# Kernel optimization log

Hardware: AMD Instinct MI355X
Metric: run time of the kernel (lower is better)

The kernel has to match this reference:

```python
import jax, jax.numpy as jnp
import numpy as np

B, T_ENC, FEAT, H, W2V, T_DEC, V = 32, 80, 4096, 256, 256, 30, 32000


def lstm_cell(x, h, c, w_ih, w_hh, b_ih, b_hh):
    # PyTorch LSTMCell: gates order i, f, g, o
    g = x @ w_ih.T + h @ w_hh.T + b_ih + b_hh
    i, f, gg, o = jnp.split(g, 4, axis=-1)
    c_new = jax.nn.sigmoid(f) * c + jax.nn.sigmoid(i) * jnp.tanh(gg)
    h_new = jax.nn.sigmoid(o) * jnp.tanh(c_new)
    return h_new, c_new


def setup_inputs() -> dict:
    key = jax.random.key(0)
    ks = jax.random.split(key, 13)
    s = 0.05
    return {
        'feat': jax.random.normal(ks[0], (B, T_ENC, FEAT), jnp.float32),
        'caption': jax.random.normal(ks[1], (B, T_DEC, W2V), jnp.float32),
        'caption_one_hot': jax.random.normal(ks[2], (B, T_DEC, V), jnp.float32),
        'keep_rate': 1,
        'w_ih1': jax.random.normal(ks[3], (4 * H, FEAT), jnp.float32) * s,
        'w_hh1': jax.random.normal(ks[4], (4 * H, H), jnp.float32) * s,
        'b_ih1': jax.random.normal(ks[5], (4 * H,), jnp.float32) * s,
        'b_hh1': jax.random.normal(ks[6], (4 * H,), jnp.float32) * s,
        'w_ih2': jax.random.normal(ks[7], (4 * H, H + W2V), jnp.float32) * s,
        'w_hh2': jax.random.normal(ks[8], (4 * H, H), jnp.float32) * s,
        'b_ih2': jax.random.normal(ks[9], (4 * H,), jnp.float32) * s,
        'b_hh2': jax.random.normal(ks[10], (4 * H,), jnp.float32) * s,
        'w_out': jax.random.normal(ks[11], (V, H), jnp.float32) * s,
        'b_out': jax.random.normal(ks[12], (V,), jnp.float32) * s,
    }


def reference(feat, caption, caption_one_hot, keep_rate,
              w_ih1, w_hh1, b_ih1, b_hh1,
              w_ih2, w_hh2, b_ih2, b_hh2,
              w_out, b_out):
    zeros_h = jnp.zeros((B, H), feat.dtype)
    pad1 = jnp.zeros((B, FEAT), feat.dtype)

    # ---------------- encoder: 80 steps ----------------
    def enc_step(carry, x_t):
        h1, c1, h2, c2 = carry
        h1, c1 = lstm_cell(x_t, h1, c1, w_ih1, w_hh1, b_ih1, b_hh1)
        h2, c2 = lstm_cell(jnp.concatenate([zeros_h, h1], axis=1), h2, c2,
                           w_ih2, w_hh2, b_ih2, b_hh2)
        return (h1, c1, h2, c2), h2

    (h1, c1, h2, c2), enc_h2 = jax.lax.scan(
        enc_step, (zeros_h, zeros_h, zeros_h, zeros_h),
        jnp.transpose(feat, (1, 0, 2)))
    enc_h2 = jnp.transpose(enc_h2, (1, 0, 2))  # [B, 80, H]

    # ---------------- decoder: teacher forcing (coin>=100 never fires) ----
    targets = jnp.argmax(caption_one_hot, axis=-1)  # [B, T_DEC]

    def dec_step(carry, xs):
        h1, c1, h2, c2, loss = carry
        word_t, tgt_t = xs  # [B, W2V], [B]
        h1, c1 = lstm_cell(pad1, h1, c1, w_ih1, w_hh1, b_ih1, b_hh1)
        h2n, c2 = lstm_cell(jnp.concatenate([word_t, h1], axis=1), h2, c2,
                            w_ih2, w_hh2, b_ih2, b_hh2)
        logits = h2n @ w_out.T + b_out  # [B, V]
        logp = jax.nn.log_softmax(logits, axis=-1)
        ce = -jnp.take_along_axis(logp, tgt_t[:, None], axis=1)[:, 0]
        loss = loss + jnp.mean(ce) / B  # sum(mean-CE)/batch, per original
        # attention: scores of encoder h2 states against current h2
        attn = jax.nn.softmax(jnp.einsum('bsh,bh->bs', enc_h2, h2n), axis=-1)
        ctx = jnp.einsum('bs,bsh->bh', attn, enc_h2)  # replaces h2 for next step
        return (h1, c1, ctx, c2, loss), None

    xs = (jnp.transpose(caption[:, :T_DEC - 1, :], (1, 0, 2)),
          jnp.transpose(targets[:, 1:T_DEC], (1, 0)))
    (h1, c1, h2, c2, total_loss), _ = jax.lax.scan(
        dec_step, (h1, c1, h2, c2, jnp.float32(0.0)), xs)
    return total_loss
```

## Files before the change

### kernel.cpp

```cpp
#include <hip/hip_runtime.h>
#include <hip/hip_bf16.h>
#include <math.h>

#define BB 32
#define TE 80
#define FEAT 4096
#define HH 256
#define W2V 256
#define TD 30
#define VV 32000
#define G4 1024

typedef unsigned short u16;
typedef unsigned int u32;
using f32x4 = __attribute__((ext_vector_type(4))) float;
using bf16x8 = __attribute__((ext_vector_type(8))) short;
using f16x2 = __attribute__((ext_vector_type(2))) _Float16;

#define SENT 0xFFFFFFFFu
#define NANF 0x7FC00000u

__device__ __forceinline__ float sigm(float x) { return 1.0f / (1.0f + expf(-x)); }
__device__ __forceinline__ u16 f2bf(float f) {
  u32 u = __float_as_uint(f);
  u32 r = (u + 0x7FFFu + ((u >> 16) & 1u)) >> 16;
  return (u16)r;
}
__device__ __forceinline__ u32 packh2(float lo, float hi) {
  f16x2 v = {(_Float16)lo, (_Float16)hi};
  return __builtin_bit_cast(u32, v);
}

#define AT_LOAD(p)     __hip_atomic_load((p), __ATOMIC_RELAXED, __HIP_MEMORY_SCOPE_AGENT)
#define AT_STORE(p, v) __hip_atomic_store((p), (v), __ATOMIC_RELAXED, __HIP_MEMORY_SCOPE_AGENT)

__device__ __forceinline__ float fdot2h(f16x2 a, f16x2 b, float c) {
#if __has_builtin(__builtin_amdgcn_fdot2)
  return __builtin_amdgcn_fdot2(a, b, c, false);
#else
  return c + (float)a[0] * (float)b[0] + (float)a[1] * (float)b[1];
#endif
}

__global__ __launch_bounds__(256) void prep_kernel(
    const float* __restrict__ feat, const float* __restrict__ w_ih1,
    const float* __restrict__ w_ih2, const float* __restrict__ caption,
    const float* __restrict__ onehot,
    const float* __restrict__ b_ih1, const float* __restrict__ b_hh1,
    const float* __restrict__ b_ih2, const float* __restrict__ b_hh2,
    u16* __restrict__ featb, u16* __restrict__ w_ih1b,
    float* __restrict__ XW2,
    float* __restrict__ bias1, float* __restrict__ bias2,
    u32* __restrict__ H1H, u32* __restrict__ H2H, u32* __restrict__ A2P,
    float* __restrict__ loss, int* __restrict__ ctrs,
    int* __restrict__ targets) {
  __shared__ __align__(16) char psm[50688];
  int blk = blockIdx.x, tid = threadIdx.x;
  if (blk < 928) {
    int k = blk;
    int s = (k >> 5) + 1, b = k & 31;
    const float* row = &onehot[((size_t)b * TD + s) * VV];
    float bv = -INFINITY;
    int bi = 0x7fffffff;
    for (int v = tid; v < VV; v += 256) {
      float x = row[v];
      if (x > bv || (x == bv && v < bi)) { bv = x; bi = v; }
    }
    float* sv = (float*)psm;
    int* si = (int*)(psm + 1024);
    sv[tid] = bv; si[tid] = bi;
    __syncthreads();
    for (int off = 128; off; off >>= 1) {
      if (tid < off) {
        float ov = sv[tid + off]; int oi = si[tid + off];
        if (ov > sv[tid] || (ov == sv[tid] && oi < si[tid])) { sv[tid] = ov; si[tid] = oi; }
      }
      __syncthreads();
    }
    if (tid == 0) targets[k] = si[0];
  } else if (blk < 3488) {
    int i0 = (blk - 928) * 1024 + tid;
#pragma unroll
    for (int ii = 0; ii < 4; ++ii) {
      int i = i0 + ii * 256;
      float4 v = *(const float4*)&feat[(size_t)i * 4];
      *(ushort4*)&featb[(size_t)i * 4] =
          make_ushort4(f2bf(v.x), f2bf(v.y), f2bf(v.z), f2bf(v.w));
    }
  } else if (blk < 4512) {
    int i0 = (blk - 3488) * 1024 + tid;
#pragma unroll
    for (int ii = 0; ii < 4; ++ii) {
      int i = i0 + ii * 256;
      float4 v = *(const float4*)&w_ih1[(size_t)i * 4];
      *(ushort4*)&w_ih1b[(size_t)i * 4] =
          make_ushort4(f2bf(v.x), f2bf(v.y), f2bf(v.z), f2bf(v.w));
    }
  } else if (blk < 4976) {
    int k = blk - 4512, nb = k & 15, t = k >> 4;
    u16* As = (u16*)psm;
    u16* Bs = (u16*)(psm + 16896);
    int nBase = nb * 64;
#pragma unroll
    for (int it = 0; it < 4; ++it) {
      int i = it * 256 + tid;
      int r = i >> 5, c8 = i & 31;
      const float* src = &caption[((size_t)r * TD + t) * 256 + c8 * 8];
      float4 v0 = *(const float4*)src;
      float4 v1 = *(const float4*)(src + 4);
      u16* dst = &As[r * 264 + c8 * 8];
      *(ushort4*)dst = make_ushort4(f2bf(v0.x), f2bf(v0.y), f2bf(v0.z), f2bf(v0.w));
      *(ushort4*)(dst + 4) = make_ushort4(f2bf(v1.x), f2bf(v1.y), f2bf(v1.z), f2bf(v1.w));
    }
#pragma unroll
    for (int it = 0; it < 8; ++it) {
      int i = it * 256 + tid;
      int r = i >> 5, c8 = i & 31;
      const float* src = &w_ih2[(size_t)(nBase + r) * 512 + c8 * 8];
      float4 v0 = *(const float4*)src;
      float4 v1 = *(const float4*)(src + 4);
      u16* dst = &Bs[r * 264 + c8 * 8];
      *(ushort4*)dst = make_ushort4(f2bf(v0.x), f2bf(v0.y), f2bf(v0.z), f2bf(v0.w));
      *(ushort4*)(dst + 4) = make_ushort4(f2bf(v1.x), f2bf(v1.y), f2bf(v1.z), f2bf(v1.w));
    }
    __syncthreads();
    int lane = tid & 63, w = tid >> 6;
    int lrow = lane & 15, lk = (lane >> 4) * 8;
    f32x4 acc[2];
    acc[0] = (f32x4){0.f, 0.f, 0.f, 0.f};
    acc[1] = (f32x4){0.f, 0.f, 0.f, 0.f};
#pragma unroll
    for (int ks = 0; ks < 8; ++ks) {
      bf16x8 bfr = *(const bf16x8*)&Bs[(w * 16 + lrow) * 264 + ks * 32 + lk];
#pragma unroll
      for (int m = 0; m < 2; ++m) {
        bf16x8 af = *(const bf16x8*)&As[(m * 16 + lrow) * 264 + ks * 32 + lk];
        acc[m] = __builtin_amdgcn_mfma_f32_16x16x32_bf16(af, bfr, acc[m], 0, 0, 0);
      }
    }
    int col = nBase + w * 16 + (lane & 15);
    float bv = b_ih2[col] + b_hh2[col];
    int orow = (lane >> 4) * 4;
#pragma unroll
    for (int m = 0; m < 2; ++m)
#pragma unroll
      for (int qq = 0; qq < 4; ++qq) {
        int bb = m * 16 + orow + qq;
        XW2[((size_t)t * 32 + bb) * G4 + col] = acc[m][qq] + bv;
      }
  } else if (blk < 5416) {
    int i = (blk - 4976) * 256 + tid;
    uint4 z = {0u, 0u, 0u, 0u};
    uint4 s = {SENT, SENT, SENT, SENT};
    uint4 v = (i < 1024) ? z : s;
    ((uint4*)H1H)[i] = v;
    ((uint4*)H2H)[i] = v;
  } else if (blk < 6296) {
    int i0 = (blk - 5416) * 1024 + tid;
    uint4 s = {NANF, NANF, NANF, NANF};
#pragma unroll
    for (int ii = 0; ii < 4; ++ii) ((uint4*)A2P)[i0 + ii * 256] = s;
  } else {
    for (int i = tid; i < 1024; i += 256) {
      bias1[i] = b_ih1[i] + b_hh1[i];
      bias2[i] = b_ih2[i] + b_hh2[i];
    }
    if (tid == 0) { *loss = 0.0f; ctrs[0] = 0; ctrs[32] = 0; }
  }
}

struct RP {
  const float *XW2, *bias1, *bias2;
  const u16 *featb, *w_ih1b;
  const float *w_hh1, *w_ih2, *w_hh2;
  u32* H1H;
  u32* H2H;
  u32* A2P;
  u16* H2NB;
};

__global__ __launch_bounds__(512, 1) void recurrent_kernel(RP p) {
  __shared__ __align__(16) char smem[133120];
  int bid = blockIdx.x, tid = threadIdx.x;
  bool isL1 = bid < 128;
  int lb = isL1 ? bid : bid - 128;
  int b = lb >> 2, q = lb & 3;
  int r2 = tid >> 1, half = tid & 1;
  int g = r2 >> 6, jj = r2 & 63;
  int grow = (g << 8) + (q << 6) + jj;

  if (isL1) {
    u16* As = (u16*)smem;
    u16* Bs = (u16*)(smem + 11520);
    float* X1L = (float*)(smem + 48384);
    f16x2* hS = (f16x2*)(smem + 130624);
    float* gb = (float*)(smem + 131136);
    float* hnew = (float*)(smem + 132160);
    {
      int lane = tid & 63, w = tid >> 6;
      int lrow = lane & 15, lk = (lane >> 4) * 8;
      f32x4 acc[5][2];
#pragma unroll
      for (int m = 0; m < 5; ++m)
#pragma unroll
        for (int n = 0; n < 2; ++n) acc[m][n] = (f32x4){0.f, 0.f, 0.f, 0.f};
      for (int k0 = 0; k0 < FEAT; k0 += 64) {
        for (int f = tid; f < 640; f += 512) {
          int r = f >> 3, c8 = f & 7;
          *(uint4*)&As[r * 72 + c8 * 8] =
              *(const uint4*)&p.featb[((size_t)(b * 80 + r)) * FEAT + k0 + c8 * 8];
        }
#pragma unroll
        for (int it = 0; it < 4; ++it) {
          int f = it * 512 + tid;
          int r = f >> 3, c8 = f & 7;
          int gg = r >> 6, u = r & 63;
          *(uint4*)&Bs[r * 72 + c8 * 8] =
              *(const uint4*)&p.w_ih1b[((size_t)(gg * 256 + q * 64 + u)) * FEAT + k0 + c8 * 8];
        }
        __syncthreads();
#pragma unroll
        for (int ks = 0; ks < 2; ++ks) {
          bf16x8 bfr[2];
#pragma unroll
          for (int n = 0; n < 2; ++n)
// ... 44 lines not shown
      b1v2 = p.bias1[512 + (q << 6) + tid];
      b1v3 = p.bias1[768 + (q << 6) + tid];
    }
    for (int T = 0; T <= 109; ++T) {
      float x0 = b1v0, x1 = b1v1, x2 = b1v2, x3 = b1v3;
      if (tid < 64 && T < TE) {
        x0 = X1L[T * 257 + tid];
        x1 = X1L[T * 257 + 64 + tid];
        x2 = X1L[T * 257 + 128 + tid];
        x3 = X1L[T * 257 + 192 + tid];
      }
      if (tid < 128) {
        const u32* src = &p.H1H[((size_t)T * 32 + b) * 128 + tid];
        u32 v = AT_LOAD(src);
        int gd = 0;
        while (v == SENT && ++gd < (1 << 24)) {
          __builtin_amdgcn_s_sleep(1);
          v = AT_LOAD(src);
        }
        hS[tid] = __builtin_bit_cast(f16x2, v);
      }
      __syncthreads();
      float a1 = 0.f, a2 = 0.f;
      {
        const uint4* hv = ((const uint4*)hS) + half * 16;
#pragma unroll
        for (int k = 0; k < 16; ++k) {
          uint4 uu = hv[k];
          f16x2 e0 = __builtin_bit_cast(f16x2, uu.x), e1 = __builtin_bit_cast(f16x2, uu.y);
          f16x2 e2 = __builtin_bit_cast(f16x2, uu.z), e3 = __builtin_bit_cast(f16x2, uu.w);
          a1 = fdot2h(e0, wA[k * 4 + 0], a1);
          a2 = fdot2h(e0, wB[k * 4 + 0], a2);
          a1 = fdot2h(e1, wA[k * 4 + 1], a1);
          a2 = fdot2h(e1, wB[k * 4 + 1], a2);
          a1 = fdot2h(e2, wA[k * 4 + 2], a1);
          a2 = fdot2h(e2, wB[k * 4 + 2], a2);
          a1 = fdot2h(e3, wA[k * 4 + 3], a1);
          a2 = fdot2h(e3, wB[k * 4 + 3], a2);
        }
      }
      a1 += __shfl_xor(a1, 1);
      a2 += __shfl_xor(a2, 1);
      if (half == 0) {
        gb[r2] = a1;
        if (T >= 1)
          AT_STORE(&p.A2P[((size_t)T * 32 + b) * 1024 + grow], __float_as_uint(a2));
      }
      __syncthreads();
      if (T <= 108) {
        if (tid < 64) {
          float gi = gb[tid] + x0;
          float gf = gb[64 + tid] + x1;
          float gG = gb[128 + tid] + x2;
          float go = gb[192 + tid] + x3;
          c1 = sigm(gf) * c1 + sigm(gi) * tanhf(gG);
          hnew[tid] = sigm(go) * tanhf(c1);
        }
        if (tid < 32) {
          u32 pk = packh2(hnew[2 * tid], hnew[2 * tid + 1]);
          AT_STORE(&p.H1H[((size_t)(T + 1) * 32 + b) * 128 + (q << 5) + tid], pk);
        }
      }
    }
  } else {
    f16x2* encLh = (f16x2*)smem;
    u16* g2Lh = (u16*)(smem + 42240);
    f16x2* hS = (f16x2*)(smem + 84480);
    float* a2pS = (float*)(smem + 85536);
    float* gb = (float*)(smem + 86560);
    float* hnew = (float*)(smem + 87584);
    float* ps = (float*)(smem + 87840);
    float* sc = (float*)(smem + 89120);
    float* red = (float*)(smem + 89440);
    f16x2 wC[64];
    {
      const float4* sC = (const float4*)(p.w_hh2 + (size_t)grow * 256 + half * 128);
#pragma unroll
      for (int k = 0; k < 32; ++k) {
        float4 u = sC[k];
        wC[k * 2 + 0] = f16x2{(_Float16)u.x, (_Float16)u.y};
        wC[k * 2 + 1] = f16x2{(_Float16)u.z, (_Float16)u.w};
      }
    }
    float c2 = 0.f;
    float b2v0 = 0, b2v1 = 0, b2v2 = 0, b2v3 = 0;
    if (tid < 64) {
      b2v0 = p.bias2[(q << 6) + tid];
      b2v1 = p.bias2[256 + (q << 6) + tid];
      b2v2 = p.bias2[512 + (q << 6) + tid];
      b2v3 = p.bias2[768 + (q << 6) + tid];
    }
    for (int U = 1; U <= 109; ++U) {
      float x0 = b2v0, x1 = b2v1, x2 = b2v2, x3 = b2v3;
      if (tid < 64 && U >= 81) {
        const float* xb = &p.XW2[((size_t)(U - 81) * 32 + b) * G4 + (q << 6) + tid];
        x0 = xb[0]; x1 = xb[256]; x2 = xb[512]; x3 = xb[768];
      }
      if (tid < 128) {
        const u32* src = &p.H2H[((size_t)(U - 1) * 32 + b) * 128 + tid];
        u32 v = AT_LOAD(src);
        int gd = 0;
        while (v == SENT && ++gd < (1 << 26)) v = AT_LOAD(src);
        f16x2 hp = __builtin_bit_cast(f16x2, v);
        hS[tid] = hp;
        if (U >= 2 && U <= 81) encLh[(U - 2) * 132 + tid] = hp;
      } else if (tid < 384) {
        int rr = tid - 128;
        int growp = ((rr >> 6) << 8) + (q << 6) + (rr & 63);
        const u32* src = &p.A2P[((size_t)U * 32 + b) * 1024 + growp];
        u32 v = AT_LOAD(src);
        int gd = 0;
        while (v == NANF && ++gd < (1 << 24)) {
          __builtin_amdgcn_s_sleep(1);
          v = AT_LOAD(src);
        }
        a2pS[rr] = __uint_as_float(v);
      }
      __syncthreads();
      float a2p0 = 0, a2p1 = 0, a2p2 = 0, a2p3 = 0;
      if (tid < 64) {
        a2p0 = a2pS[tid]; a2p1 = a2pS[64 + tid];
        a2p2 = a2pS[128 + tid]; a2p3 = a2pS[192 + tid];
      }
      if (U <= 81) {
        float a2 = 0.f;
        const uint4* hv = ((const uint4*)hS) + half * 16;
#pragma unroll
        for (int k = 0; k < 16; ++k) {
          uint4 uu = hv[k];
          a2 = fdot2h(__builtin_bit_cast(f16x2, uu.x), wC[k * 4 + 0], a2);
          a2 = fdot2h(__builtin_bit_cast(f16x2, uu.y), wC[k * 4 + 1], a2);
          a2 = fdot2h(__builtin_bit_cast(f16x2, uu.z), wC[k * 4 + 2], a2);
          a2 = fdot2h(__builtin_bit_cast(f16x2, uu.w), wC[k * 4 + 3], a2);
        }
        a2 += __shfl_xor(a2, 1);
        if (half == 0) {
          gb[r2] = a2;
          if (U >= 2) g2Lh[(U - 2) * 264 + r2] = __builtin_bit_cast(u16, (_Float16)a2);
        }
        __syncthreads();
      } else {
        if (tid < 320) {
          int t = tid >> 2, kq = tid & 3;
          float a = 0.f;
          const f16x2* e = &encLh[t * 132];
#pragma unroll
          for (int i = 0; i < 32; ++i)
            a = fdot2h(e[kq + 4 * i], hS[kq + 4 * i], a);
          ps[tid] = a;
        }
        __syncthreads();
        float sco = 0.f;
        if (tid < TE) sco = ps[4 * tid] + ps[4 * tid + 1] + ps[4 * tid + 2] + ps[4 * tid + 3];
        float av = (tid < TE) ? sco : -INFINITY;
#pragma unroll
        for (int d = 32; d; d >>= 1) av = fmaxf(av, __shfl_xor(av, d));
        if (tid == 0) red[0] = av;
        if (tid == 64) red[1] = av;
        __syncthreads();
        float m = fmaxf(red[0], red[1]);
        float e2 = (tid < TE) ? expf(sco - m) : 0.f;
        float sv = e2;
#pragma unroll
// ... 11 lines not shown
          float g2v = (float)__builtin_bit_cast(_Float16, g2Lh[t * 264 + r2]);
          acc = fmaf(sc[t], g2v, acc);
        }
        acc += __shfl_xor(acc, 1);
        if (half == 0) gb[r2] = acc;
        __syncthreads();
      }
      if (tid < 64) {
        float gi = gb[tid] + a2p0 + x0;
        float gf = gb[64 + tid] + a2p1 + x1;
        float gG = gb[128 + tid] + a2p2 + x2;
        float go = gb[192 + tid] + a2p3 + x3;
        c2 = sigm(gf) * c2 + sigm(gi) * tanhf(gG);
        float h = sigm(go) * tanhf(c2);
        hnew[tid] = h;
        if (U >= 81)
          p.H2NB[((size_t)(U - 81) * 32 + b) * 256 + (q << 6) + tid] = f2bf(h);
      }
      if (tid < 32) {
        u32 pk = packh2(hnew[2 * tid], hnew[2 * tid + 1]);
        AT_STORE(&p.H2H[((size_t)U * 32 + b) * 128 + (q << 5) + tid], pk);
      }
    }
  }
}

__global__ __launch_bounds__(256, 1) void logits_final_kernel(
    const u16* __restrict__ H2NB, const float* __restrict__ w_out,
    const float* __restrict__ b_out, const int* __restrict__ targets,
    u32* __restrict__ pmaxA, u32* __restrict__ psumA, u32* __restrict__ tgtv,
    float* __restrict__ loss, int* __restrict__ ctrs, float* __restrict__ out) {
  __shared__ __align__(16) u16 bS[32768];
  __shared__ __align__(16) u16 aS[32 * 264];
  __shared__ int tS[32];
  __shared__ float sm[256];
  int tid = threadIdx.x, bid = blockIdx.x;
#pragma unroll
  for (int it = 0; it < 16; ++it) {
    int id = it * 256 + tid;
    int nt = id >> 9, rr = (id >> 5) & 15, kg = id & 31;
    int n = bid * 128 + nt * 16 + rr;
    const float* src = &w_out[(size_t)n * 256 + kg * 8];
    float4 v0 = *(const float4*)src;
    float4 v1 = *(const float4*)(src + 4);
    u16* dst = &bS[(size_t)((nt * 32 + kg) * 16 + rr) * 8];
    *(ushort4*)dst = make_ushort4(f2bf(v0.x), f2bf(v0.y), f2bf(v0.z), f2bf(v0.w));
    *(ushort4*)(dst + 4) = make_ushort4(f2bf(v1.x), f2bf(v1.y), f2bf(v1.z), f2bf(v1.w));
  }
  int wid = tid >> 6, lane = tid & 63, lcol = lane & 15, lk = lane >> 4;
  float bo[2];
#pragma unroll
  for (int n = 0; n < 2; ++n) bo[n] = b_out[(bid * 8 + wid * 2 + n) * 16 + lcol];

  for (int rg = 0; rg < 29; ++rg) {
    __syncthreads();
    for (int i = tid; i < 1024; i += 256) {
      int r = i >> 5, c8 = i & 31;
      *(uint4*)&aS[r * 264 + c8 * 8] =
          *(const uint4*)&H2NB[(size_t)rg * 8192 + r * 256 + c8 * 8];
    }
    if (tid < 32) tS[tid] = targets[rg * 32 + tid];
    __syncthreads();
    f32x4 acc[2][2];
#pragma unroll
    for (int m = 0; m < 2; ++m)
#pragma unroll
      for (int n = 0; n < 2; ++n) acc[m][n] = (f32x4){0.f, 0.f, 0.f, 0.f};
#pragma unroll
    for (int ks = 0; ks < 8; ++ks) {
      bf16x8 a0 = *(const bf16x8*)&aS[lcol * 264 + ks * 32 + lk * 8];
      bf16x8 a1 = *(const bf16x8*)&aS[(16 + lcol) * 264 + ks * 32 + lk * 8];
      bf16x8 b0 = *(const bf16x8*)&bS[(wid * 2) * 4096 + ((ks * 4 + lk) * 16 + lcol) * 8];
      bf16x8 b1 = *(const bf16x8*)&bS[(wid * 2 + 1) * 4096 + ((ks * 4 + lk) * 16 + lcol) * 8];
      acc[0][0] = __builtin_amdgcn_mfma_f32_16x16x32_bf16(a0, b0, acc[0][0], 0, 0, 0);
      acc[0][1] = __builtin_amdgcn_mfma_f32_16x16x32_bf16(a0, b1, acc[0][1], 0, 0, 0);
      acc[1][0] = __builtin_amdgcn_mfma_f32_16x16x32_bf16(a1, b0, acc[1][0], 0, 0, 0);
      acc[1][1] = __builtin_amdgcn_mfma_f32_16x16x32_bf16(a1, b1, acc[1][1], 0, 0, 0);
    }
    int nbase = (bid * 8 + wid * 2) * 16 + lcol;
#pragma unroll
    for (int m = 0; m < 2; ++m) {
      float pm[4], psv[4];
#pragma unroll
      for (int qq = 0; qq < 4; ++qq) {
        float v0 = acc[m][0][qq] + bo[0];
        float v1 = acc[m][1][qq] + bo[1];
        int r = m * 16 + lk * 4 + qq;
        int tg = tS[r];
        if (tg == nbase) AT_STORE(&tgtv[rg * 32 + r], __float_as_uint(v0));
        if (tg == nbase + 16) AT_STORE(&tgtv[rg * 32 + r], __float_as_uint(v1));
        float mx = fmaxf(v0, v1);
#pragma unroll
        for (int d = 1; d < 16; d <<= 1) mx = fmaxf(mx, __shfl_xor(mx, d));
        float e = expf(v0 - mx) + expf(v1 - mx);
#pragma unroll
        for (int d = 1; d < 16; d <<= 1) e += __shfl_xor(e, d);
        pm[qq] = mx;
        psv[qq] = e;
      }
      if (lcol == 0) {
        int chunk = bid * 4 + wid;
#pragma unroll
        for (int qq = 0; qq < 4; ++qq) {
          int r2 = rg * 32 + m * 16 + lk * 4 + qq;
          AT_STORE(&pmaxA[(size_t)r2 * 1000 + chunk], __float_as_uint(pm[qq]));
          AT_STORE(&psumA[(size_t)r2 * 1000 + chunk], __float_as_uint(psv[qq]));
        }
      }
    }
  }
  asm volatile("s_waitcnt vmcnt(0)" ::: "memory");
  __syncthreads();
  if (tid == 0) {
    __hip_atomic_fetch_add(&ctrs[0], 1, __ATOMIC_RELEASE, __HIP_MEMORY_SCOPE_AGENT);
    int gd = 0;
    while (__hip_atomic_load(&ctrs[0], __ATOMIC_ACQUIRE, __HIP_MEMORY_SCOPE_AGENT) < 250 &&
           ++gd < (1 << 26))
      __builtin_amdgcn_s_sleep(2);
  }
  __syncthreads();
#pragma unroll
  for (int k = 0; k < 4; ++k) {
    int row = bid * 4 + k;
    if (row < 928) {
      const u32* pm = pmaxA + (size_t)row * 1000;
      const u32* psv = psumA + (size_t)row * 1000;
      float m = -INFINITY;
      for (int c = tid; c < 1000; c += 256) m = fmaxf(m, __uint_as_float(AT_LOAD(&pm[c])));
      sm[tid] = m;
      __syncthreads();
      for (int off = 128; off; off >>= 1) {
        if (tid < off) sm[tid] = fmaxf(sm[tid], sm[tid + off]);
        __syncthreads();
      }
      float M = sm[0];
      __syncthreads();
      float s = 0.f;
      for (int c = tid; c < 1000; c += 256)
        s += __uint_as_float(AT_LOAD(&psv[c])) * expf(__uint_as_float(AT_LOAD(&pm[c])) - M);
      sm[tid] = s;
      __syncthreads();
      for (int off = 128; off; off >>= 1) {
        if (tid < off) sm[tid] += sm[tid + off];
        __syncthreads();
      }
      if (tid == 0) {
        float tv = __uint_as_float(AT_LOAD(&tgtv[row]));
        atomicAdd(loss, (M + logf(sm[0]) - tv) * (1.0f / 1024.0f));
      }
      __syncthreads();
    }
  }
  asm volatile("s_waitcnt vmcnt(0)" ::: "memory");
  if (tid == 0) {
    int old = __hip_atomic_fetch_add(&ctrs[32], 1, __ATOMIC_ACQ_REL, __HIP_MEMORY_SCOPE_AGENT);
    if (old == 249) out[0] = __uint_as_float(AT_LOAD((u32*)loss));
  }
}

extern "C" void kernel_launch(void* const* d_in, const int* in_sizes, int n_in,
                              void* d_out, int out_size, void* d_ws, size_t ws_size,
                              hipStream_t stream) {
  (void)in_sizes; (void)n_in; (void)out_size; (void)ws_size;
  const float* feat    = (const float*)d_in[0];
  const float* caption = (const float*)d_in[1];
  const float* onehot  = (const float*)d_in[2];
  const float* w_ih1   = (const float*)d_in[4];
  const float* w_hh1   = (const float*)d_in[5];
  const float* b_ih1   = (const float*)d_in[6];
  const float* b_hh1   = (const float*)d_in[7];
  const float* w_ih2   = (const float*)d_in[8];
  const float* w_hh2   = (const float*)d_in[9];
  const float* b_ih2   = (const float*)d_in[10];
  const float* b_hh2   = (const float*)d_in[11];
  const float* w_out   = (const float*)d_in[12];
  const float* b_out   = (const float*)d_in[13];

  char* p = (char*)d_ws;
  auto alloc = [&](size_t bytes) {
    char* r = p;
    p += (bytes + 255) & ~(size_t)255;
    return r;
  };
  float* XW2     = (float*)alloc(29ull * 32 * 1024 * 4);
  float* bias1   = (float*)alloc(1024 * 4);
  float* bias2   = (float*)alloc(1024 * 4);
  u32*   H1H     = (u32*)alloc(110ull * 32 * 128 * 4);
  u32*   H2H     = (u32*)alloc(110ull * 32 * 128 * 4);
  u32*   A2P     = (u32*)alloc(110ull * 32 * 1024 * 4);
  u16*   H2NB    = (u16*)alloc(29ull * 8192 * 2);
  u32*   pmaxA   = (u32*)alloc(928ull * 1000 * 4);
  u32*   psumA   = (u32*)alloc(928ull * 1000 * 4);
  u32*   tgtv    = (u32*)alloc(928 * 4);
  float* lossacc = (float*)alloc(256);
  int*   ctrs    = (int*)alloc(256);
  int*   targets = (int*)alloc(29 * 32 * 4);
  u16*   featb   = (u16*)alloc(2560ull * 4096 * 2);
  u16*   w_ih1b  = (u16*)alloc(1024ull * 4096 * 2);

  prep_kernel<<<6297, 256, 0, stream>>>(
      feat, w_ih1, w_ih2, caption, onehot,
      b_ih1, b_hh1, b_ih2, b_hh2,
      featb, w_ih1b, XW2,
      bias1, bias2, H1H, H2H, A2P, lossacc, ctrs, targets);

  RP rp;
  rp.XW2 = XW2; rp.bias1 = bias1; rp.bias2 = bias2;
  rp.featb = featb; rp.w_ih1b = w_ih1b;
  rp.w_hh1 = w_hh1; rp.w_ih2 = w_ih2; rp.w_hh2 = w_hh2;
  rp.H1H = H1H; rp.H2H = H2H; rp.A2P = A2P; rp.H2NB = H2NB;
  void* args[] = {&rp};
  hipLaunchCooperativeKernel((const void*)recurrent_kernel, dim3(256), dim3(512),
                             args, 0, stream);

  logits_final_kernel<<<250, 256, 0, stream>>>(H2NB, w_out, b_out, targets,
                                               pmaxA, psumA, tgtv, lossacc, ctrs,
                                               (float*)d_out);
}
```

Measured before the change: 704.1 us.

## Fuse argmax, input projections and logits into the cooperative recurrent mega-kernel

Folds the target argmax, the caption input projection (XW2), the feature bf16 conversion and the logits/log-softmax stage into the persistent cooperative kernel. The logits now run per step while the decoder is still progressing, driven by work queues and per-step counters. The A2P exchange is halved by packing two values as fp16 pairs, and the prep kernel shrinks to weight conversion and buffer initialisation. This removes a separate kernel launch, the featb round trip through global memory and the serial tail after the recurrence. In exchange it adds spin-wait dependencies and per-block work inside the recurrent kernel, which can delay the critical-path timesteps.

```diff
diff --git a/kernel.cpp b/kernel.cpp
--- a/kernel.cpp
+++ b/kernel.cpp
@@ -18,7 +18,7 @@
 using f16x2 = __attribute__((ext_vector_type(2))) _Float16;
 
 #define SENT 0xFFFFFFFFu
-#define NANF 0x7FC00000u
+#define GUARD (1 << 22)
 
 __device__ __forceinline__ float sigm(float x) { return 1.0f / (1.0f + expf(-x)); }
 __device__ __forceinline__ u16 f2bf(float f) {
@@ -30,9 +30,13 @@
   f16x2 v = {(_Float16)lo, (_Float16)hi};
   return __builtin_bit_cast(u32, v);
 }
+__device__ __forceinline__ u32 packbf2(float lo, float hi) {
+  return (u32)f2bf(lo) | ((u32)f2bf(hi) << 16);
+}
 
 #define AT_LOAD(p)     __hip_atomic_load((p), __ATOMIC_RELAXED, __HIP_MEMORY_SCOPE_AGENT)
 #define AT_STORE(p, v) __hip_atomic_store((p), (v), __ATOMIC_RELAXED, __HIP_MEMORY_SCOPE_AGENT)
+#define AT_ADD(p, v)   __hip_atomic_fetch_add((p), (v), __ATOMIC_RELAXED, __HIP_MEMORY_SCOPE_AGENT)
 
 __device__ __forceinline__ float fdot2h(f16x2 a, f16x2 b, float c) {
 #if __has_builtin(__builtin_amdgcn_fdot2)
@@ -42,53 +46,24 @@
 #endif
 }
 
+#define C_BAR 0
+#define C_WRT 32
+#define C_ARGQ 64
+#define C_ARGD 72
+#define C_CHQ 96
+#define C_RG 128
+
 __global__ __launch_bounds__(256) void prep_kernel(
-    const float* __restrict__ feat, const float* __restrict__ w_ih1,
-    const float* __restrict__ w_ih2, const float* __restrict__ caption,
-    const float* __restrict__ onehot,
+    const float* __restrict__ w_ih1,
     const float* __restrict__ b_ih1, const float* __restrict__ b_hh1,
     const float* __restrict__ b_ih2, const float* __restrict__ b_hh2,
-    u16* __restrict__ featb, u16* __restrict__ w_ih1b,
-    float* __restrict__ XW2,
+    u16* __restrict__ w_ih1b,
     float* __restrict__ bias1, float* __restrict__ bias2,
     u32* __restrict__ H1H, u32* __restrict__ H2H, u32* __restrict__ A2P,
-    float* __restrict__ loss, int* __restrict__ ctrs,
-    int* __restrict__ targets) {
-  __shared__ __align__(16) char psm[50688];
+    float* __restrict__ loss, int* __restrict__ ctrs) {
   int blk = blockIdx.x, tid = threadIdx.x;
-  if (blk < 928) {
-    int k = blk;
-    int s = (k >> 5) + 1, b = k & 31;
-    const float* row = &onehot[((size_t)b * TD + s) * VV];
-    float bv = -INFINITY;
-    int bi = 0x7fffffff;
-    for (int v = tid; v < VV; v += 256) {
-      float x = row[v];
-      if (x > bv || (x == bv && v < bi)) { bv = x; bi = v; }
-    }
-    float* sv = (float*)psm;
-    int* si = (int*)(psm + 1024);
-    sv[tid] = bv; si[tid] = bi;
-    __syncthreads();
-    for (int off = 128; off; off >>= 1) {
-      if (tid < off) {
-        float ov = sv[tid + off]; int oi = si[tid + off];
-        if (ov > sv[tid] || (ov == sv[tid] && oi < si[tid])) { sv[tid] = ov; si[tid] = oi; }
-      }
-      __syncthreads();
-    }
-    if (tid == 0) targets[k] = si[0];
-  } else if (blk < 3488) {
-    int i0 = (blk - 928) * 1024 + tid;
-#pragma unroll
-    for (int ii = 0; ii < 4; ++ii) {
-      int i = i0 + ii * 256;
-      float4 v = *(const float4*)&feat[(size_t)i * 4];
-      *(ushort4*)&featb[(size_t)i * 4] =
-          make_ushort4(f2bf(v.x), f2bf(v.y), f2bf(v.z), f2bf(v.w));
-    }
-  } else if (blk < 4512) {
-    int i0 = (blk - 3488) * 1024 + tid;
+  if (blk < 1024) {
+    int i0 = blk * 1024 + tid;
 #pragma unroll
     for (int ii = 0; ii < 4; ++ii) {
       int i = i0 + ii * 256;
@@ -96,68 +71,16 @@
       *(ushort4*)&w_ih1b[(size_t)i * 4] =
           make_ushort4(f2bf(v.x), f2bf(v.y), f2bf(v.z), f2bf(v.w));
     }
-  } else if (blk < 4976) {
-    int k = blk - 4512, nb = k & 15, t = k >> 4;
-    u16* As = (u16*)psm;
-    u16* Bs = (u16*)(psm + 16896);
-    int nBase = nb * 64;
-#pragma unroll
-    for (int it = 0; it < 4; ++it) {
-      int i = it * 256 + tid;
-      int r = i >> 5, c8 = i & 31;
-      const float* src = &caption[((size_t)r * TD + t) * 256 + c8 * 8];
-      float4 v0 = *(const float4*)src;
-      float4 v1 = *(const float4*)(src + 4);
-      u16* dst = &As[r * 264 + c8 * 8];
-      *(ushort4*)dst = make_ushort4(f2bf(v0.x), f2bf(v0.y), f2bf(v0.z), f2bf(v0.w));
-      *(ushort4*)(dst + 4) = make_ushort4(f2bf(v1.x), f2bf(v1.y), f2bf(v1.z), f2bf(v1.w));
-    }
-#pragma unroll
-    for (int it = 0; it < 8; ++it) {
-      int i = it * 256 + tid;
-      int r = i >> 5, c8 = i & 31;
-      const float* src = &w_ih2[(size_t)(nBase + r) * 512 + c8 * 8];
-      float4 v0 = *(const float4*)src;
-      float4 v1 = *(const float4*)(src + 4);
-      u16* dst = &Bs[r * 264 + c8 * 8];
-      *(ushort4*)dst = make_ushort4(f2bf(v0.x), f2bf(v0.y), f2bf(v0.z), f2bf(v0.w));
-      *(ushort4*)(dst + 4) = make_ushort4(f2bf(v1.x), f2bf(v1.y), f2bf(v1.z), f2bf(v1.w));
-    }
-    __syncthreads();
-    int lane = tid & 63, w = tid >> 6;
-    int lrow = lane & 15, lk = (lane >> 4) * 8;
-    f32x4 acc[2];
-    acc[0] = (f32x4){0.f, 0.f, 0.f, 0.f};
-    acc[1] = (f32x4){0.f, 0.f, 0.f, 0.f};
-#pragma unroll
-    for (int ks = 0; ks < 8; ++ks) {
-      bf16x8 bfr = *(const bf16x8*)&Bs[(w * 16 + lrow) * 264 + ks * 32 + lk];
-#pragma unroll
-      for (int m = 0; m < 2; ++m) {
-        bf16x8 af = *(const bf16x8*)&As[(m * 16 + lrow) * 264 + ks * 32 + lk];
-        acc[m] = __builtin_amdgcn_mfma_f32_16x16x32_bf16(af, bfr, acc[m], 0, 0, 0);
-      }
-    }
-    int col = nBase + w * 16 + (lane & 15);
-    float bv = b_ih2[col] + b_hh2[col];
-    int orow = (lane >> 4) * 4;
-#pragma unroll
-    for (int m = 0; m < 2; ++m)
-#pragma unroll
-      for (int qq = 0; qq < 4; ++qq) {
-        int bb = m * 16 + orow + qq;
-        XW2[((size_t)t * 32 + bb) * G4 + col] = acc[m][qq] + bv;
-      }
-  } else if (blk < 5416) {
-    int i = (blk - 4976) * 256 + tid;
+  } else if (blk < 1464) {
+    int i = (blk - 1024) * 256 + tid;
     uint4 z = {0u, 0u, 0u, 0u};
     uint4 s = {SENT, SENT, SENT, SENT};
     uint4 v = (i < 1024) ? z : s;
     ((uint4*)H1H)[i] = v;
     ((uint4*)H2H)[i] = v;
-  } else if (blk < 6296) {
-    int i0 = (blk - 5416) * 1024 + tid;
-    uint4 s = {NANF, NANF, NANF, NANF};
+  } else if (blk < 1904) {
+    int i0 = (blk - 1464) * 1024 + tid;
+    uint4 s = {SENT, SENT, SENT, SENT};
 #pragma unroll
     for (int ii = 0; ii < 4; ++ii) ((uint4*)A2P)[i0 + ii * 256] = s;
   } else {
@@ -165,21 +88,118 @@
       bias1[i] = b_ih1[i] + b_hh1[i];
       bias2[i] = b_ih2[i] + b_hh2[i];
     }
-    if (tid == 0) { *loss = 0.0f; ctrs[0] = 0; ctrs[32] = 0; }
+    if (tid < 256) ctrs[tid] = 0;
+    if (tid == 0) *loss = 0.0f;
   }
 }
 
 struct RP {
-  const float *XW2, *bias1, *bias2;
-  const u16 *featb, *w_ih1b;
-  const float *w_hh1, *w_ih2, *w_hh2;
+  const float *feat, *caption, *onehot;
+  const float *w_hh1, *w_ih2, *w_hh2, *w_out, *b_out;
+  const float *bias1, *bias2;
+  const u16* w_ih1b;
   u32* H1H;
   u32* H2H;
   u32* A2P;
-  u16* H2NB;
+  u32* H2NB32;
+  u32 *pmaxA, *psumA, *tgtv;
+  float* loss;
+  int* ctrs;
+  int* targets;
+  float* out;
 };
 
-__global__ __launch_bounds__(512, 1) void recurrent_kernel(RP p) {
+__device__ void do_logits(char* smem, const RP& p) {
+  u16* bS = (u16*)smem;
+  u16* aS = (u16*)(smem + 65536);
+  int* tS = (int*)(smem + 82432);
+  int* chS = (int*)(smem + 82560);
+  int tid = threadIdx.x;
+  if (tid == 0) {
+    int gd = 0;
+    while (AT_LOAD(&p.ctrs[C_ARGD]) < 928 && ++gd < GUARD) __builtin_amdgcn_s_sleep(2);
+  }
+  __syncthreads();
+  int w = tid >> 6, lane = tid & 63, lcol = lane & 15, lk = lane >> 4;
+  while (true) {
+    if (tid == 0) *chS = AT_ADD(&p.ctrs[C_CHQ], 1);
+    __syncthreads();
+    int ch = *chS;
+    if (ch >= 250) break;
+#pragma unroll
+    for (int it = 0; it < 8; ++it) {
+      int id = it * 512 + tid;
+      int nt = id >> 9, rr = (id >> 5) & 15, kg = id & 31;
+      int n = ch * 128 + nt * 16 + rr;
+      const float* src = &p.w_out[(size_t)n * 256 + kg * 8];
+      float4 v0 = *(const float4*)src;
+      float4 v1 = *(const float4*)(src + 4);
+      u16* dst = &bS[(size_t)((nt * 32 + kg) * 16 + rr) * 8];
+      *(ushort4*)dst = make_ushort4(f2bf(v0.x), f2bf(v0.y), f2bf(v0.z), f2bf(v0.w));
+      *(ushort4*)(dst + 4) = make_ushort4(f2bf(v1.x), f2bf(v1.y), f2bf(v1.z), f2bf(v1.w));
+    }
+    float bo = p.b_out[ch * 128 + w * 16 + lcol];
+    for (int rg = 0; rg < 29; ++rg) {
+      if (tid == 0) {
+        int gd = 0;
+        while (AT_LOAD(&p.ctrs[C_RG + rg]) < 128 && ++gd < GUARD) __builtin_amdgcn_s_sleep(1);
+      }
+      __syncthreads();
+#pragma unroll
+      for (int it = 0; it < 8; ++it) {
+        int i = it * 512 + tid;
+        int r = i >> 7, cu = i & 127;
+        u32 v = AT_LOAD(&p.H2NB32[((size_t)rg * 32 + r) * 128 + cu]);
+        aS[r * 264 + cu * 2] = (u16)(v & 0xFFFF);
+        aS[r * 264 + cu * 2 + 1] = (u16)(v >> 16);
+      }
+      if (tid < 32) tS[tid] = AT_LOAD(&p.targets[rg * 32 + tid]);
+      __syncthreads();
+      f32x4 acc[2];
+      acc[0] = (f32x4){0.f, 0.f, 0.f, 0.f};
+      acc[1] = (f32x4){0.f, 0.f, 0.f, 0.f};
+#pragma unroll
+      for (int ks = 0; ks < 8; ++ks) {
+        bf16x8 bfr = *(const bf16x8*)&bS[(size_t)((w * 32 + ks * 4 + lk) * 16 + lcol) * 8];
+        bf16x8 a0 = *(const bf16x8*)&aS[lcol * 264 + ks * 32 + lk * 8];
+        bf16x8 a1 = *(const bf16x8*)&aS[(16 + lcol) * 264 + ks * 32 + lk * 8];
+        acc[0] = __builtin_amdgcn_mfma_f32_16x16x32_bf16(a0, bfr, acc[0], 0, 0, 0);
+        acc[1] = __builtin_amdgcn_mfma_f32_16x16x32_bf16(a1, bfr, acc[1], 0, 0, 0);
+      }
+      int ncol = ch * 128 + w * 16 + lcol;
+      int chunkW = ch * 8 + w;
+#pragma unroll
+      for (int m = 0; m < 2; ++m) {
+        float pm[4], psv[4];
+#pragma unroll
+        for (int qq = 0; qq < 4; ++qq) {
+          float v0 = acc[m][qq] + bo;
+          int r = m * 16 + lk * 4 + qq;
+          if (tS[r] == ncol) AT_STORE(&p.tgtv[rg * 32 + r], __float_as_uint(v0));
+          float mx = v0;
+#pragma unroll
+          for (int d = 1; d < 16; d <<= 1) mx = fmaxf(mx, __shfl_xor(mx, d));
+          float e = expf(v0 - mx);
+#pragma unroll
+          for (int d = 1; d < 16; d <<= 1) e += __shfl_xor(e, d);
+          pm[qq] = mx;
+          psv[qq] = e;
+        }
+        if (lcol == 0) {
+#pragma unroll
+          for (int qq = 0; qq < 4; ++qq) {
+            int r2 = (rg * 32 + m * 16 + lk * 4 + qq);
+            AT_STORE(&p.pmaxA[(size_t)r2 * 2000 + chunkW], __float_as_uint(pm[qq]));
+            AT_STORE(&p.psumA[(size_t)r2 * 2000 + chunkW], __float_as_uint(psv[qq]));
+          }
+        }
+      }
+      __syncthreads();
+    }
+  }
+}
+
+__global__ __launch_bounds__(512, 1) void mega_kernel(RP p) {
   __shared__ __align__(16) char smem[133120];
   int bid = blockIdx.x, tid = threadIdx.x;
   bool isL1 = bid < 128;
@@ -205,10 +225,11 @@
 #pragma unroll
         for (int n = 0; n < 2; ++n) acc[m][n] = (f32x4){0.f, 0.f, 0.f, 0.f};
       for (int k0 = 0; k0 < FEAT; k0 += 64) {
-        for (int f = tid; f < 640; f += 512) {
-          int r = f >> 3, c8 = f & 7;
-          *(uint4*)&As[r * 72 + c8 * 8] =
-              *(const uint4*)&p.featb[((size_t)(b * 80 + r)) * FEAT + k0 + c8 * 8];
+        for (int f = tid; f < 1280; f += 512) {
+          int r = f >> 4, c4 = f & 15;
+          float4 v = *(const float4*)&p.feat[((size_t)(b * 80 + r)) * FEAT + k0 + c4 * 4];
+          *(ushort4*)&As[r * 72 + c4 * 4] =
+              make_ushort4(f2bf(v.x), f2bf(v.y), f2bf(v.z), f2bf(v.w));
         }
 #pragma unroll
         for (int it = 0; it < 4; ++it) {
@@ -283,7 +304,7 @@
         const u32* src = &p.H1H[((size_t)T * 32 + b) * 128 + tid];
         u32 v = AT_LOAD(src);
         int gd = 0;
-        while (v == SENT && ++gd < (1 << 24)) {
+        while (v == SENT && ++gd < GUARD) {
           __builtin_amdgcn_s_sleep(1);
           v = AT_LOAD(src);
         }
@@ -310,10 +331,13 @@
       }
       a1 += __shfl_xor(a1, 1);
       a2 += __shfl_xor(a2, 1);
-      if (half == 0) {
-        gb[r2] = a1;
-        if (T >= 1)
-          AT_STORE(&p.A2P[((size_t)T * 32 + b) * 1024 + grow], __float_as_uint(a2));
+      float a2o = __shfl_xor(a2, 2);
+      if (half == 0) gb[r2] = a1;
+      if ((tid & 3) == 0 && T >= 1) {
+        int pr = tid >> 2;
+        int gp = pr >> 5, wp = pr & 31;
+        AT_STORE(&p.A2P[((size_t)T * 32 + b) * 512 + (gp << 7) + (q << 5) + wp],
+                 packh2(a2, a2o));
       }
       __syncthreads();
       if (T <= 108) {
@@ -331,16 +355,98 @@
         }
       }
     }
+    {
+      float* sv = (float*)smem;
+      int* si = (int*)(smem + 2048);
+      int* jobS = (int*)(smem + 4096);
+      __syncthreads();
+      while (true) {
+        if (tid == 0) *jobS = AT_ADD(&p.ctrs[C_ARGQ], 1);
+        __syncthreads();
+        int job = *jobS;
+        if (job >= 928) break;
+        int s = (job >> 5) + 1, bb = job & 31;
+        const float* row = &p.onehot[((size_t)bb * TD + s) * VV];
+        float bv = -INFINITY;
+        int bi = 0x7fffffff;
+        for (int v = tid; v < VV; v += 512) {
+          float x = row[v];
+          if (x > bv || (x == bv && v < bi)) { bv = x; bi = v; }
+        }
+        sv[tid] = bv;
+        si[tid] = bi;
+        __syncthreads();
+        for (int off = 256; off; off >>= 1) {
+          if (tid < off) {
+            float ov = sv[tid + off];
+            int oi = si[tid + off];
+            if (ov > sv[tid] || (ov == sv[tid] && oi < si[tid])) { sv[tid] = ov; si[tid] = oi; }
+          }
+          __syncthreads();
+        }
+        if (tid == 0) {
+          AT_STORE(&p.targets[job], si[0]);
+          asm volatile("s_waitcnt vmcnt(0)" ::: "memory");
+          AT_ADD(&p.ctrs[C_ARGD], 1);
+        }
+        __syncthreads();
+      }
+    }
+    do_logits(smem, p);
   } else {
     f16x2* encLh = (f16x2*)smem;
     u16* g2Lh = (u16*)(smem + 42240);
-    f16x2* hS = (f16x2*)(smem + 84480);
-    float* a2pS = (float*)(smem + 85536);
-    float* gb = (float*)(smem + 86560);
-    float* hnew = (float*)(smem + 87584);
-    float* ps = (float*)(smem + 87840);
-    float* sc = (float*)(smem + 89120);
-    float* red = (float*)(smem + 89440);
+    float* XW2L = (float*)(smem + 84480);
+    f16x2* hS = (f16x2*)(smem + 115136);
+    float* a2pS = (float*)(smem + 115648);
+    float* gb = (float*)(smem + 116672);
+    float* hnew = (float*)(smem + 117696);
+    float* ps = (float*)(smem + 117952);
+    float* sc = (float*)(smem + 119232);
+    float* red = (float*)(smem + 119552);
+    {
+      u16* pAs = (u16*)smem;
+      u16* pBs = (u16*)(smem + 16896);
+      for (int f = tid; f < 2048; f += 512) {
+        int r = f >> 6, c = f & 63;
+        ushort4 o = make_ushort4(0, 0, 0, 0);
+        if (r < 29) {
+          float4 v = *(const float4*)&p.caption[((size_t)b * TD + r) * 256 + c * 4];
+          o = make_ushort4(f2bf(v.x), f2bf(v.y), f2bf(v.z), f2bf(v.w));
+        }
+        *(ushort4*)&pAs[r * 264 + c * 4] = o;
+      }
+      int lane = tid & 63, w = tid >> 6;
+      int m = w >> 2, n = w & 3;
+      int lrow = lane & 15, lk = (lane >> 4) * 8;
+      for (int g2 = 0; g2 < 4; ++g2) {
+#pragma unroll
+        for (int it = 0; it < 8; ++it) {
+          int f = it * 512 + tid;
+          int r = f >> 6, c = f & 63;
+          float4 v = *(const float4*)&p.w_ih2[((size_t)(g2 * 256 + q * 64 + r)) * 512 + c * 4];
+          *(ushort4*)&pBs[r * 264 + c * 4] =
+              make_ushort4(f2bf(v.x), f2bf(v.y), f2bf(v.z), f2bf(v.w));
+        }
+        __syncthreads();
+        f32x4 acc = (f32x4){0.f, 0.f, 0.f, 0.f};
+#pragma unroll
+        for (int ks = 0; ks < 8; ++ks) {
+          bf16x8 af = *(const bf16x8*)&pAs[(m * 16 + lrow) * 264 + ks * 32 + lk];
+          bf16x8 bfr = *(const bf16x8*)&pBs[(n * 16 + lrow) * 264 + ks * 32 + lk];
+          acc = __builtin_amdgcn_mfma_f32_16x16x32_bf16(af, bfr, acc, 0, 0, 0);
+        }
+        int lcol = lane & 15, orow = (lane >> 4) * 4;
+        int u = n * 16 + lcol;
+        float bv = p.bias2[g2 * 256 + q * 64 + u];
+#pragma unroll
+        for (int qq = 0; qq < 4; ++qq) {
+          int s = m * 16 + orow + qq;
+          if (s < 29) XW2L[s * 264 + g2 * 64 + u] = acc[qq] + bv;
+        }
+        __syncthreads();
+      }
+    }
     f16x2 wC[64];
     {
       const float4* sC = (const float4*)(p.w_hh2 + (size_t)grow * 256 + half * 128);
@@ -362,34 +468,41 @@
     for (int U = 1; U <= 109; ++U) {
       float x0 = b2v0, x1 = b2v1, x2 = b2v2, x3 = b2v3;
       if (tid < 64 && U >= 81) {
-        const float* xb = &p.XW2[((size_t)(U - 81) * 32 + b) * G4 + (q << 6) + tid];
-        x0 = xb[0]; x1 = xb[256]; x2 = xb[512]; x3 = xb[768];
+        int s = U - 81;
+        x0 = XW2L[s * 264 + tid];
+        x1 = XW2L[s * 264 + 64 + tid];
+        x2 = XW2L[s * 264 + 128 + tid];
+        x3 = XW2L[s * 264 + 192 + tid];
       }
       if (tid < 128) {
         const u32* src = &p.H2H[((size_t)(U - 1) * 32 + b) * 128 + tid];
         u32 v = AT_LOAD(src);
         int gd = 0;
-        while (v == SENT && ++gd < (1 << 26)) v = AT_LOAD(src);
+        while (v == SENT && ++gd < (GUARD << 2)) v = AT_LOAD(src);
         f16x2 hp = __builtin_bit_cast(f16x2, v);
         hS[tid] = hp;
         if (U >= 2 && U <= 81) encLh[(U - 2) * 132 + tid] = hp;
-      } else if (tid < 384) {
+      } else if (tid < 256) {
         int rr = tid - 128;
-        int growp = ((rr >> 6) << 8) + (q << 6) + (rr & 63);
-        const u32* src = &p.A2P[((size_t)U * 32 + b) * 1024 + growp];
+        int gp = rr >> 5, wp = rr & 31;
+        const u32* src = &p.A2P[((size_t)U * 32 + b) * 512 + (gp << 7) + (q << 5) + wp];
         u32 v = AT_LOAD(src);
         int gd = 0;
-        while (v == NANF && ++gd < (1 << 24)) {
+        while (v == SENT && ++gd < GUARD) {
           __builtin_amdgcn_s_sleep(1);
           v = AT_LOAD(src);
         }
-        a2pS[rr] = __uint_as_float(v);
+        f16x2 pr = __builtin_bit_cast(f16x2, v);
+        a2pS[gp * 64 + 2 * wp] = (float)pr[0];
+        a2pS[gp * 64 + 2 * wp + 1] = (float)pr[1];
       }
       __syncthreads();
       float a2p0 = 0, a2p1 = 0, a2p2 = 0, a2p3 = 0;
       if (tid < 64) {
-        a2p0 = a2pS[tid]; a2p1 = a2pS[64 + tid];
-        a2p2 = a2pS[128 + tid]; a2p3 = a2pS[192 + tid];
+        a2p0 = a2pS[tid];
+        a2p1 = a2pS[64 + tid];
+        a2p2 = a2pS[128 + tid];
+        a2p3 = a2pS[192 + tid];
       }
       if (U <= 81) {
         float a2 = 0.f;
@@ -414,8 +527,7 @@
           float a = 0.f;
           const f16x2* e = &encLh[t * 132];
 #pragma unroll
-          for (int i = 0; i < 32; ++i)
-            a = fdot2h(e[kq + 4 * i], hS[kq + 4 * i], a);
+          for (int i = 0; i < 32; ++i) a = fdot2h(e[kq + 4 * i], hS[kq + 4 * i], a);
           ps[tid] = a;
         }
         __syncthreads();
@@ -457,147 +569,73 @@
         c2 = sigm(gf) * c2 + sigm(gi) * tanhf(gG);
         float h = sigm(go) * tanhf(c2);
         hnew[tid] = h;
-        if (U >= 81)
-          p.H2NB[((size_t)(U - 81) * 32 + b) * 256 + (q << 6) + tid] = f2bf(h);
       }
       if (tid < 32) {
         u32 pk = packh2(hnew[2 * tid], hnew[2 * tid + 1]);
         AT_STORE(&p.H2H[((size_t)U * 32 + b) * 128 + (q << 5) + tid], pk);
-      }
-    }
-  }
-}
-
-__global__ __launch_bounds__(256, 1) void logits_final_kernel(
-    const u16* __restrict__ H2NB, const float* __restrict__ w_out,
-    const float* __restrict__ b_out, const int* __restrict__ targets,
-    u32* __restrict__ pmaxA, u32* __restrict__ psumA, u32* __restrict__ tgtv,
-    float* __restrict__ loss, int* __restrict__ ctrs, float* __restrict__ out) {
-  __shared__ __align__(16) u16 bS[32768];
-  __shared__ __align__(16) u16 aS[32 * 264];
-  __shared__ int tS[32];
-  __shared__ float sm[256];
-  int tid = threadIdx.x, bid = blockIdx.x;
-#pragma unroll
-  for (int it = 0; it < 16; ++it) {
-    int id = it * 256 + tid;
-    int nt = id >> 9, rr = (id >> 5) & 15, kg = id & 31;
-    int n = bid * 128 + nt * 16 + rr;
-    const float* src = &w_out[(size_t)n * 256 + kg * 8];
-    float4 v0 = *(const float4*)src;
-    float4 v1 = *(const float4*)(src + 4);
-    u16* dst = &bS[(size_t)((nt * 32 + kg) * 16 + rr) * 8];
-    *(ushort4*)dst = make_ushort4(f2bf(v0.x), f2bf(v0.y), f2bf(v0.z), f2bf(v0.w));
-    *(ushort4*)(dst + 4) = make_ushort4(f2bf(v1.x), f2bf(v1.y), f2bf(v1.z), f2bf(v1.w));
-  }
-  int wid = tid >> 6, lane = tid & 63, lcol = lane & 15, lk = lane >> 4;
-  float bo[2];
-#pragma unroll
-  for (int n = 0; n < 2; ++n) bo[n] = b_out[(bid * 8 + wid * 2 + n) * 16 + lcol];
-
-  for (int rg = 0; rg < 29; ++rg) {
+        if (U >= 81) {
+          int rg = U - 81;
+          u32 bk = packbf2(hnew[2 * tid], hnew[2 * tid + 1]);
+          AT_STORE(&p.H2NB32[((size_t)rg * 32 + b) * 128 + (q << 5) + tid], bk);
+        }
+      }
+      if (U >= 81) {
+        asm volatile("s_waitcnt vmcnt(0)" ::: "memory");
+        if (tid == 0) AT_ADD(&p.ctrs[C_RG + (U - 81)], 1);
+      }
+    }
     __syncthreads();
-    for (int i = tid; i < 1024; i += 256) {
-      int r = i >> 5, c8 = i & 31;
-      *(uint4*)&aS[r * 264 + c8 * 8] =
-          *(const uint4*)&H2NB[(size_t)rg * 8192 + r * 256 + c8 * 8];
-    }
-    if (tid < 32) tS[tid] = targets[rg * 32 + tid];
-    __syncthreads();
-    f32x4 acc[2][2];
-#pragma unroll
-    for (int m = 0; m < 2; ++m)
-#pragma unroll
-      for (int n = 0; n < 2; ++n) acc[m][n] = (f32x4){0.f, 0.f, 0.f, 0.f};
-#pragma unroll
-    for (int ks = 0; ks < 8; ++ks) {
-      bf16x8 a0 = *(const bf16x8*)&aS[lcol * 264 + ks * 32 + lk * 8];
-      bf16x8 a1 = *(const bf16x8*)&aS[(16 + lcol) * 264 + ks * 32 + lk * 8];
-      bf16x8 b0 = *(const bf16x8*)&bS[(wid * 2) * 4096 + ((ks * 4 + lk) * 16 + lcol) * 8];
-      bf16x8 b1 = *(const bf16x8*)&bS[(wid * 2 + 1) * 4096 + ((ks * 4 + lk) * 16 + lcol) * 8];
-      acc[0][0] = __builtin_amdgcn_mfma_f32_16x16x32_bf16(a0, b0, acc[0][0], 0, 0, 0);
-      acc[0][1] = __builtin_amdgcn_mfma_f32_16x16x32_bf16(a0, b1, acc[0][1], 0, 0, 0);
-      acc[1][0] = __builtin_amdgcn_mfma_f32_16x16x32_bf16(a1, b0, acc[1][0], 0, 0, 0);
-      acc[1][1] = __builtin_amdgcn_mfma_f32_16x16x32_bf16(a1, b1, acc[1][1], 0, 0, 0);
-    }
-    int nbase = (bid * 8 + wid * 2) * 16 + lcol;
-#pragma unroll
-    for (int m = 0; m < 2; ++m) {
-      float pm[4], psv[4];
-#pragma unroll
-      for (int qq = 0; qq < 4; ++qq) {
-        float v0 = acc[m][0][qq] + bo[0];
-        float v1 = acc[m][1][qq] + bo[1];
-        int r = m * 16 + lk * 4 + qq;
-        int tg = tS[r];
-        if (tg == nbase) AT_STORE(&tgtv[rg * 32 + r], __float_as_uint(v0));
-        if (tg == nbase + 16) AT_STORE(&tgtv[rg * 32 + r], __float_as_uint(v1));
-        float mx = fmaxf(v0, v1);
-#pragma unroll
-        for (int d = 1; d < 16; d <<= 1) mx = fmaxf(mx, __shfl_xor(mx, d));
-        float e = expf(v0 - mx) + expf(v1 - mx);
-#pragma unroll
-        for (int d = 1; d < 16; d <<= 1) e += __shfl_xor(e, d);
-        pm[qq] = mx;
-        psv[qq] = e;
-      }
-      if (lcol == 0) {
-        int chunk = bid * 4 + wid;
-#pragma unroll
-        for (int qq = 0; qq < 4; ++qq) {
-          int r2 = rg * 32 + m * 16 + lk * 4 + qq;
-          AT_STORE(&pmaxA[(size_t)r2 * 1000 + chunk], __float_as_uint(pm[qq]));
-          AT_STORE(&psumA[(size_t)r2 * 1000 + chunk], __float_as_uint(psv[qq]));
-        }
-      }
-    }
+    do_logits(smem, p);
   }
   asm volatile("s_waitcnt vmcnt(0)" ::: "memory");
   __syncthreads();
   if (tid == 0) {
-    __hip_atomic_fetch_add(&ctrs[0], 1, __ATOMIC_RELEASE, __HIP_MEMORY_SCOPE_AGENT);
+    __hip_atomic_fetch_add(&p.ctrs[C_BAR], 1, __ATOMIC_RELEASE, __HIP_MEMORY_SCOPE_AGENT);
     int gd = 0;
-    while (__hip_atomic_load(&ctrs[0], __ATOMIC_ACQUIRE, __HIP_MEMORY_SCOPE_AGENT) < 250 &&
-           ++gd < (1 << 26))
+    while (__hip_atomic_load(&p.ctrs[C_BAR], __ATOMIC_ACQUIRE, __HIP_MEMORY_SCOPE_AGENT) < 256 &&
+           ++gd < GUARD)
       __builtin_amdgcn_s_sleep(2);
   }
   __syncthreads();
-#pragma unroll
-  for (int k = 0; k < 4; ++k) {
-    int row = bid * 4 + k;
-    if (row < 928) {
-      const u32* pm = pmaxA + (size_t)row * 1000;
-      const u32* psv = psumA + (size_t)row * 1000;
-      float m = -INFINITY;
-      for (int c = tid; c < 1000; c += 256) m = fmaxf(m, __uint_as_float(AT_LOAD(&pm[c])));
-      sm[tid] = m;
-      __syncthreads();
-      for (int off = 128; off; off >>= 1) {
-        if (tid < off) sm[tid] = fmaxf(sm[tid], sm[tid + off]);
-        __syncthreads();
-      }
-      float M = sm[0];
-      __syncthreads();
-      float s = 0.f;
-      for (int c = tid; c < 1000; c += 256)
-        s += __uint_as_float(AT_LOAD(&psv[c])) * expf(__uint_as_float(AT_LOAD(&pm[c])) - M);
-      sm[tid] = s;
-      __syncthreads();
-      for (int off = 128; off; off >>= 1) {
-        if (tid < off) sm[tid] += sm[tid + off];
-        __syncthreads();
-      }
-      if (tid == 0) {
-        float tv = __uint_as_float(AT_LOAD(&tgtv[row]));
-        atomicAdd(loss, (M + logf(sm[0]) - tv) * (1.0f / 1024.0f));
-      }
-      __syncthreads();
+  {
+    float* sm = (float*)smem;
+#pragma unroll
+    for (int k = 0; k < 4; ++k) {
+      int row = bid * 4 + k;
+      if (row < 928) {
+        const u32* pm = p.pmaxA + (size_t)row * 2000;
+        const u32* psv = p.psumA + (size_t)row * 2000;
+        float m = -INFINITY;
+        for (int c = tid; c < 2000; c += 512) m = fmaxf(m, __uint_as_float(AT_LOAD(&pm[c])));
+        sm[tid] = m;
+        __syncthreads();
+        for (int off = 256; off; off >>= 1) {
+          if (tid < off) sm[tid] = fmaxf(sm[tid], sm[tid + off]);
+          __syncthreads();
+        }
+        float M = sm[0];
+        __syncthreads();
+        float s = 0.f;
+        for (int c = tid; c < 2000; c += 512)
+          s += __uint_as_float(AT_LOAD(&psv[c])) * expf(__uint_as_float(AT_LOAD(&pm[c])) - M);
+        sm[tid] = s;
+        __syncthreads();
+        for (int off = 256; off; off >>= 1) {
+          if (tid < off) sm[tid] += sm[tid + off];
+          __syncthreads();
+        }
+        if (tid == 0) {
+          float tv = __uint_as_float(AT_LOAD(&p.tgtv[row]));
+          atomicAdd(p.loss, (M + logf(sm[0]) - tv) * (1.0f / 1024.0f));
+        }
+        __syncthreads();
+      }
     }
   }
   asm volatile("s_waitcnt vmcnt(0)" ::: "memory");
   if (tid == 0) {
-    int old = __hip_atomic_fetch_add(&ctrs[32], 1, __ATOMIC_ACQ_REL, __HIP_MEMORY_SCOPE_AGENT);
-    if (old == 249) out[0] = __uint_as_float(AT_LOAD((u32*)loss));
+    int old = __hip_atomic_fetch_add(&p.ctrs[C_WRT], 1, __ATOMIC_ACQ_REL, __HIP_MEMORY_SCOPE_AGENT);
+    if (old == 255) p.out[0] = __uint_as_float(AT_LOAD((u32*)p.loss));
   }
 }
 
@@ -625,38 +663,34 @@
     p += (bytes + 255) & ~(size_t)255;
     return r;
   };
-  float* XW2     = (float*)alloc(29ull * 32 * 1024 * 4);
   float* bias1   = (float*)alloc(1024 * 4);
   float* bias2   = (float*)alloc(1024 * 4);
   u32*   H1H     = (u32*)alloc(110ull * 32 * 128 * 4);
   u32*   H2H     = (u32*)alloc(110ull * 32 * 128 * 4);
-  u32*   A2P     = (u32*)alloc(110ull * 32 * 1024 * 4);
-  u16*   H2NB    = (u16*)alloc(29ull * 8192 * 2);
-  u32*   pmaxA   = (u32*)alloc(928ull * 1000 * 4);
-  u32*   psumA   = (u32*)alloc(928ull * 1000 * 4);
+  u32*   A2P     = (u32*)alloc(110ull * 32 * 512 * 4);
+  u32*   H2NB32  = (u32*)alloc(29ull * 32 * 128 * 4);
+  u32*   pmaxA   = (u32*)alloc(928ull * 2000 * 4);
+  u32*   psumA   = (u32*)alloc(928ull * 2000 * 4);
   u32*   tgtv    = (u32*)alloc(928 * 4);
   float* lossacc = (float*)alloc(256);
-  int*   ctrs    = (int*)alloc(256);
+  int*   ctrs    = (int*)alloc(1024);
   int*   targets = (int*)alloc(29 * 32 * 4);
-  u16*   featb   = (u16*)alloc(2560ull * 4096 * 2);
   u16*   w_ih1b  = (u16*)alloc(1024ull * 4096 * 2);
 
-  prep_kernel<<<6297, 256, 0, stream>>>(
-      feat, w_ih1, w_ih2, caption, onehot,
-      b_ih1, b_hh1, b_ih2, b_hh2,
-      featb, w_ih1b, XW2,
-      bias1, bias2, H1H, H2H, A2P, lossacc, ctrs, targets);
+  prep_kernel<<<1905, 256, 0, stream>>>(
+      w_ih1, b_ih1, b_hh1, b_ih2, b_hh2,
+      w_ih1b, bias1, bias2, H1H, H2H, A2P, lossacc, ctrs);
 
   RP rp;
-  rp.XW2 = XW2; rp.bias1 = bias1; rp.bias2 = bias2;
-  rp.featb = featb; rp.w_ih1b = w_ih1b;
+  rp.feat = feat; rp.caption = caption; rp.onehot = onehot;
   rp.w_hh1 = w_hh1; rp.w_ih2 = w_ih2; rp.w_hh2 = w_hh2;
-  rp.H1H = H1H; rp.H2H = H2H; rp.A2P = A2P; rp.H2NB = H2NB;
+  rp.w_out = w_out; rp.b_out = b_out;
+  rp.bias1 = bias1; rp.bias2 = bias2; rp.w_ih1b = w_ih1b;
+  rp.H1H = H1H; rp.H2H = H2H; rp.A2P = A2P; rp.H2NB32 = H2NB32;
+  rp.pmaxA = pmaxA; rp.psumA = psumA; rp.tgtv = tgtv;
+  rp.loss = lossacc; rp.ctrs = ctrs; rp.targets = targets;
+  rp.out = (float*)d_out;
   void* args[] = {&rp};
-  hipLaunchCooperativeKernel((const void*)recurrent_kernel, dim3(256), dim3(512),
+  hipLaunchCooperativeKernel((const void*)mega_kernel, dim3(256), dim3(512),
                              args, 0, stream);
-
-  logits_final_kernel<<<250, 256, 0, stream>>>(H2NB, w_out, b_out, targets,
-                                               pmaxA, psumA, tgtv, lossacc, ctrs,
-                                               (float*)d_out);
-}
+}
```

Result: slower. 802.0 us (+13.9%).
